# Optimization experiments

Hardware: AMD Instinct MI355X
Metric: run time of the kernel (lower is better)

Reference implementation:

```python
import jax, jax.numpy as jnp
import numpy as np

N = 100000   # points in input set
K = 1024     # num centroids AND max neighbors per ball (as in original code)
C = 64       # input feature channels
R = 0.2      # ball radius
LAYERS = (64, 64, 128)


def setup_inputs() -> dict:
    key = jax.random.key(0)
    ks = jax.random.split(key, 9)
    coords = jax.random.uniform(ks[0], (N, 3), dtype=jnp.float32)
    features = jax.random.normal(ks[1], (N, C), dtype=jnp.float32)
    centroid_idx = jax.random.randint(ks[2], (K,), 0, N)
    dims = (3 + C,) + LAYERS
    params = {}
    for i in range(len(LAYERS)):
        fin, fout = dims[i], dims[i + 1]
        params[f"W{i+1}"] = (jax.random.normal(ks[3 + i], (fin, fout), dtype=jnp.float32)
                             / np.float32(np.sqrt(fin)))
        params[f"b{i+1}"] = jax.random.normal(ks[6 + i], (fout,), dtype=jnp.float32) * 0.01
    return dict(coords=coords, features=features, centroid_idx=centroid_idx, **params)


def reference(coords, features, centroid_idx, W1, b1, W2, b2, W3, b3):
    cent = coords[centroid_idx]                                   # [K,3]
    # squared distances [K,N] without materializing [K,N,3]
    d2 = (jnp.sum(cent * cent, axis=-1)[:, None]
          + jnp.sum(coords * coords, axis=-1)[None, :]
          - 2.0 * cent @ coords.T)
    mask = d2 <= R * R                                            # ball query
    # take the FIRST K in-radius points in original index order (matches [:K])
    rank = jnp.cumsum(mask.astype(jnp.int32), axis=1) - 1
    sel = mask & (rank < K)
    order = jnp.where(sel, jnp.arange(N)[None, :], N)
    idx = jnp.sort(order, axis=1)[:, :K]                          # [K,K]
    valid = idx < N
    idx_c = jnp.minimum(idx, N - 1)
    rel = coords[idx_c] - cent[:, None, :]                        # centered coords
    x = jnp.concatenate([rel, features[idx_c]], axis=-1)          # [K,K,3+C]
    for W, b in ((W1, b1), (W2, b2), (W3, b3)):
        x = jax.nn.relu(x @ W + b)
    x = jnp.where(valid[:, :, None], x, -jnp.inf)
    new_features = jnp.max(x, axis=1)                             # per-region max pool
    return cent, new_features
```

## Files before the change

kernel.cpp:

```cpp
#include <hip/hip_runtime.h>
#include <hip/hip_bf16.h>

#define NPTS    100000
#define KCENT   1024
#define NSEG    391
#define NWORDS  1564
#define WSTRIDE 1600
#define MB_BLKS (NSEG*32)

typedef __attribute__((ext_vector_type(8))) short bf16x8;
typedef __attribute__((ext_vector_type(4))) float f32x4;
typedef unsigned long long u64;

__device__ __forceinline__ unsigned short f2bf(float x) {
  union { float f; unsigned u; } v; v.f = x;
  unsigned r = v.u + 0x7FFFu + ((v.u >> 16) & 1u);
  return (unsigned short)(r >> 16);
}
__device__ __forceinline__ unsigned pk2bf(float a, float b) {
  union { __hip_bfloat162 h; unsigned u; } cv;
  cv.h = __float22bfloat162_rn(make_float2(a, b));
  return cv.u;
}
__device__ __forceinline__ bf16x8 pack_bf8(f32x4 a, f32x4 b) {
  union { bf16x8 v; unsigned u[4]; } r;
  r.u[0] = pk2bf(a[0], a[1]); r.u[1] = pk2bf(a[2], a[3]);
  r.u[2] = pk2bf(b[0], b[1]); r.u[3] = pk2bf(b[2], b[3]);
  return r.v;
}

__global__ __launch_bounds__(256) void build_prep_kernel(
    const float* __restrict__ coords, const float* __restrict__ features,
    const int* __restrict__ cidx, const float* __restrict__ W1,
    const float* __restrict__ b1, const float* __restrict__ W2,
    const float* __restrict__ W3, u64* __restrict__ maskbuf,
    unsigned short* __restrict__ featsBF, f32x4* __restrict__ coords4,
    unsigned short* __restrict__ W1T, unsigned short* __restrict__ W2T,
    unsigned short* __restrict__ W3T, float* __restrict__ outCent) {
  const int bid = blockIdx.x;
  const int tid = threadIdx.x;
  if (bid < MB_BLKS) {
    const int grp = bid / NSEG, seg = bid - grp*NSEG;
    __shared__ float sC[96];
    __shared__ float sCC[32];
    if (tid < 96) sC[tid] = coords[cidx[grp*32 + tid/3]*3 + tid%3];
    __syncthreads();
    if (tid < 32) {
      float x = sC[tid*3], y = sC[tid*3+1], z = sC[tid*3+2];
      sCC[tid] = __fadd_rn(__fadd_rn(__fmul_rn(x,x), __fmul_rn(y,y)), __fmul_rn(z,z));
    }
    const int p = seg*256 + tid;
    const bool inr = p < NPTS;
    float px = 0.f, py = 0.f, pz = 0.f;
    if (inr) { px = coords[p*3]; py = coords[p*3+1]; pz = coords[p*3+2]; }
    const float pp = __fadd_rn(__fadd_rn(__fmul_rn(px,px), __fmul_rn(py,py)), __fmul_rn(pz,pz));
    __syncthreads();
    const int lane = tid & 63, wid = tid >> 6;
    u64 myw = 0ull;
    #pragma unroll
    for (int ci = 0; ci < 32; ++ci) {
      float cx = sC[ci*3], cy = sC[ci*3+1], cz = sC[ci*3+2];
      float dt = __fadd_rn(__fadd_rn(__fmul_rn(cx,px), __fmul_rn(cy,py)), __fmul_rn(cz,pz));
      float d2 = __fsub_rn(__fadd_rn(sCC[ci], pp), __fmul_rn(2.0f, dt));
      bool sel = inr && (d2 <= 0.04f);
      u64 m = __ballot(sel);
      if (lane == ci) myw = m;
    }
    if (lane < 32)
      maskbuf[(u64)(grp*32 + lane)*WSTRIDE + seg*4 + wid] = myw;
    return;
  }
  int i = (bid - MB_BLKS) * 256 + tid;
  if (i < 800000) {
    const f32x4* src = (const f32x4*)features + i*2;
    f32x4 f0 = src[0], f1 = src[1];
    union { bf16x8 v; uint4 u; } pk; pk.v = pack_bf8(f0, f1);
    ((uint4*)featsBF)[i] = pk.u;
    return;
  }
  i -= 800000;
  if (i < NPTS) {
    coords4[i] = (f32x4){coords[3*i], coords[3*i+1], coords[3*i+2], 0.f};
    return;
  }
  i -= NPTS;
  if (i < 6144) {
    int n = i / 96, kk = i - n*96;
    float v = 0.f;
    if (kk < 64)       v = W1[(3+kk)*64 + n];
    else if (kk < 67)  v = W1[(kk-64)*64 + n];
    else if (kk == 67) v = b1[n];
    W1T[n*96 + kk] = f2bf(v);
    return;
  }
  i -= 6144;
  if (i < 4608) { int n = i / 72, kk = i - n*72;
    W2T[n*72 + kk] = f2bf(kk < 64 ? W2[kk*64 + n] : 0.f); return; }
  i -= 4608;
  if (i < 9216) { int n = i / 72, kk = i - n*72;
    W3T[n*72 + kk] = f2bf(kk < 64 ? W3[kk*128 + n] : 0.f); return; }
  i -= 9216;
  if (i < KCENT) {
    int ci = cidx[i];
    outCent[i*3+0] = coords[ci*3+0];
    outCent[i*3+1] = coords[ci*3+1];
    outCent[i*3+2] = coords[ci*3+2];
  }
}

__global__ __launch_bounds__(256, 2) void fused_kernel(
    const u64* __restrict__ maskbuf, const unsigned short* __restrict__ featsBF,
    const f32x4* __restrict__ coords4, const float* __restrict__ cent,
    const float* __restrict__ b2v, const float* __restrict__ b3v,
    const unsigned short* __restrict__ gW1T, const unsigned short* __restrict__ gW2T,
    const unsigned short* __restrict__ gW3T, float* __restrict__ outF) {
  __shared__ __align__(16) unsigned short sW2T[64*72];
  __shared__ __align__(16) unsigned short sH[4*2*16*72];
  __shared__ int sIdx[KCENT];
  __shared__ int sTot[4];
  __shared__ float sB2[64], sB3[128];
  __shared__ float sMax[512];

  const int k = blockIdx.x;
  const int tid = threadIdx.x;
  const int w = tid >> 6, lane = tid & 63;
  const int q = lane >> 4, cl = lane & 15;

  const u64* M = maskbuf + (u64)k * WSTRIDE;
  u64 wv0 = M[tid], wv1 = M[256 + tid], wv2 = M[512 + tid];

  for (int i = tid; i < 576; i += 256) ((uint4*)sW2T)[i] = ((const uint4*)gW2T)[i];
  if (tid < 64)  sB2[tid] = b2v[tid];
  if (tid < 128) sB3[tid] = b3v[tid];

  bf16x8 w1f[3][4], w3f[2][8];
  #pragma unroll
  for (int ks = 0; ks < 3; ++ks)
    #pragma unroll
    for (int nt = 0; nt < 4; ++nt)
      w1f[ks][nt] = *(const bf16x8*)(gW1T + (nt*16+cl)*96 + ks*32 + q*8);
  #pragma unroll
  for (int ks = 0; ks < 2; ++ks)
    #pragma unroll
    for (int nt = 0; nt < 8; ++nt)
      w3f[ks][nt] = *(const bf16x8*)(gW3T + (nt*16+cl)*72 + ks*32 + q*8);

  int base = 0;
  #pragma unroll 1
  for (int r = 0; r < 7; ++r) {
    const int widx = r*256 + tid;
    u64 word = (r == 0) ? wv0 : (r == 1) ? wv1 : (r == 2) ? wv2
             : ((widx < NWORDS) ? M[widx] : 0ull);
    int pc = __popcll(word);
    int inc = pc;
    #pragma unroll
    for (int d = 1; d < 64; d <<= 1) {
      int t = __shfl_up(inc, d);
      if (lane >= d) inc += t;
    }
    if (lane == 63) sTot[w] = inc;
    __syncthreads();
    int wbase = 0, tot = 0;
    #pragma unroll
    for (int i = 0; i < 4; ++i) { int v = sTot[i]; tot += v; if (i < w) wbase += v; }
    int pos = base + wbase + inc - pc;
    const int pbase = widx * 64;
    while (word != 0ull && pos < KCENT) {
      int b = __ffsll(word) - 1;
      sIdx[pos++] = pbase + b;
      word &= word - 1ull;
    }
    base += tot;
    __syncthreads();
    if (base >= KCENT) break;
  }
  const int count = base < KCENT ? base : KCENT;

  const float cx = cent[k*3], cy = cent[k*3+1], cz = cent[k*3+2];
  unsigned short* myHA = sH + w*2304;
  unsigned short* myHB = myHA + 1152;

  f32x4 runmax[8];
  #pragma unroll
  for (int i = 0; i < 8; ++i)
    runmax[i] = (f32x4){-__builtin_inff(), -__builtin_inff(),
                        -__builtin_inff(), -__builtin_inff()};

  const int nstrips = (count + 15) >> 4;
  const int npairs  = (nstrips + 1) >> 1;
  int pp = w;

  int pA = 0, pB = 0;
  { int jA = 32*pp + cl;      if (jA < count) pA = sIdx[jA];
    int jB = 32*pp + 16 + cl; if (jB < count) pB = sIdx[jB]; }
  f32x4  c4A = coords4[pA], c4B = coords4[pB];
  bf16x8 xfA0 = *(const bf16x8*)(featsBF + pA*64 + q*8);
  bf16x8 xfA1 = *(const bf16x8*)(featsBF + pA*64 + 32 + q*8);
  bf16x8 xfB0 = *(const bf16x8*)(featsBF + pB*64 + q*8);
  bf16x8 xfB1 = *(const bf16x8*)(featsBF + pB*64 + 32 + q*8);
  int pA2 = 0, pB2 = 0;
  { int jA = 32*(pp+4) + cl;      if (jA < count) pA2 = sIdx[jA];
    int jB = 32*(pp+4) + 16 + cl; if (jB < count) pB2 = sIdx[jB]; }

  const bf16x8 zero8 = (bf16x8){0,0,0,0,0,0,0,0};

  for (; pp < npairs; pp += 4) {
    int pA3 = 0, pB3 = 0;
    { int jA = 32*(pp+8) + cl;      if (jA < count) pA3 = sIdx[jA];
      int jB = 32*(pp+8) + 16 + cl; if (jB < count) pB3 = sIdx[jB]; }

    union { bf16x8 v; unsigned u[4]; } rfA, rfB;
    rfA.u[0] = pk2bf(c4A[0]-cx, c4A[1]-cy); rfA.u[1] = pk2bf(c4A[2]-cz, 1.0f);
    rfA.u[2] = 0u; rfA.u[3] = 0u;
    rfB.u[0] = pk2bf(c4B[0]-cx, c4B[1]-cy); rfB.u[1] = pk2bf(c4B[2]-cz, 1.0f);
    rfB.u[2] = 0u; rfB.u[3] = 0u;
    bf16x8 x2A = (q == 0) ? rfA.v : zero8;
    bf16x8 x2B = (q == 0) ? rfB.v : zero8;

    {
      f32x4 accA[4], accB[4];
      #pragma unroll
      for (int nt = 0; nt < 4; ++nt) { accA[nt] = (f32x4){0.f,0.f,0.f,0.f};
                                       accB[nt] = (f32x4){0.f,0.f,0.f,0.f}; }
      #pragma unroll
      for (int nt = 0; nt < 4; ++nt) {
        accA[nt] = __builtin_amdgcn_mfma_f32_16x16x32_bf16(w1f[0][nt], xfA0, accA[nt], 0,0,0);
        accB[nt] = __builtin_amdgcn_mfma_f32_16x16x32_bf16(w1f[0][nt], xfB0, accB[nt], 0,0,0);
      }
      #pragma unroll
      for (int nt = 0; nt < 4; ++nt) {
        accA[nt] = __builtin_amdgcn_mfma_f32_16x16x32_bf16(w1f[1][nt], xfA1, accA[nt], 0,0,0);
        accB[nt] = __builtin_amdgcn_mfma_f32_16x16x32_bf16(w1f[1][nt], xfB1, accB[nt], 0,0,0);
      }
      #pragma unroll
      for (int nt = 0; nt < 4; ++nt) {
        accA[nt] = __builtin_amdgcn_mfma_f32_16x16x32_bf16(w1f[2][nt], x2A, accA[nt], 0,0,0);
        accB[nt] = __builtin_amdgcn_mfma_f32_16x16x32_bf16(w1f[2][nt], x2B, accB[nt], 0,0,0);
      }
      #pragma unroll
      for (int nt = 0; nt < 4; ++nt) {
        const int o = nt*16 + q*4;
        uint2 pkA = { pk2bf(fmaxf(accA[nt][0],0.f), fmaxf(accA[nt][1],0.f)),
                      pk2bf(fmaxf(accA[nt][2],0.f), fmaxf(accA[nt][3],0.f)) };
        *(uint2*)(myHA + cl*72 + o) = pkA;
        uint2 pkB = { pk2bf(fmaxf(accB[nt][0],0.f), fmaxf(accB[nt][1],0.f)),
                      pk2bf(fmaxf(accB[nt][2],0.f), fmaxf(accB[nt][3],0.f)) };
        *(uint2*)(myHB + cl*72 + o) = pkB;
      }
    }

    c4A = coords4[pA2]; c4B = coords4[pB2];
    xfA0 = *(const bf16x8*)(featsBF + pA2*64 + q*8);
    xfA1 = *(const bf16x8*)(featsBF + pA2*64 + 32 + q*8);
    xfB0 = *(const bf16x8*)(featsBF + pB2*64 + q*8);
    xfB1 = *(const bf16x8*)(featsBF + pB2*64 + 32 + q*8);

    {
      bf16x8 hA0 = *(const bf16x8*)(myHA + cl*72 + q*8);
      bf16x8 hA1 = *(const bf16x8*)(myHA + cl*72 + 32 + q*8);
      bf16x8 hB0 = *(const bf16x8*)(myHB + cl*72 + q*8);
      bf16x8 hB1 = *(const bf16x8*)(myHB + cl*72 + 32 + q*8);
      f32x4 accA[4], accB[4];
      #pragma unroll
      for (int nt = 0; nt < 4; ++nt) { accA[nt] = (f32x4){0.f,0.f,0.f,0.f};
                                       accB[nt] = (f32x4){0.f,0.f,0.f,0.f}; }
      #pragma unroll
      for (int nt = 0; nt < 4; ++nt) {
        const unsigned short* wrow = sW2T + (nt*16+cl)*72 + q*8;
        bf16x8 wa0 = *(const bf16x8*)(wrow);
        accA[nt] = __builtin_amdgcn_mfma_f32_16x16x32_bf16(wa0, hA0, accA[nt], 0,0,0);
        accB[nt] = __builtin_amdgcn_mfma_f32_16x16x32_bf16(wa0, hB0, accB[nt], 0,0,0);
        bf16x8 wa1 = *(const bf16x8*)(wrow + 32);
        accA[nt] = __builtin_amdgcn_mfma_f32_16x16x32_bf16(wa1, hA1, accA[nt], 0,0,0);
        accB[nt] = __builtin_amdgcn_mfma_f32_16x16x32_bf16(wa1, hB1, accB[nt], 0,0,0);
      }
      #pragma unroll
      for (int nt = 0; nt < 4; ++nt) {
        const int o = nt*16 + q*4;
        f32x4 bb = *(const f32x4*)(sB2 + o);
        uint2 pkA = { pk2bf(fmaxf(accA[nt][0]+bb[0],0.f), fmaxf(accA[nt][1]+bb[1],0.f)),
                      pk2bf(fmaxf(accA[nt][2]+bb[2],0.f), fmaxf(accA[nt][3]+bb[3],0.f)) };
        *(uint2*)(myHA + cl*72 + o) = pkA;
        uint2 pkB = { pk2bf(fmaxf(accB[nt][0]+bb[0],0.f), fmaxf(accB[nt][1]+bb[1],0.f)),
                      pk2bf(fmaxf(accB[nt][2]+bb[2],0.f), fmaxf(accB[nt][3]+bb[3],0.f)) };
        *(uint2*)(myHB + cl*72 + o) = pkB;
      }
    }

    {
      bf16x8 hA0 = *(const bf16x8*)(myHA + cl*72 + q*8);
      bf16x8 hA1 = *(const bf16x8*)(myHA + cl*72 + 32 + q*8);
      bf16x8 hB0 = *(const bf16x8*)(myHB + cl*72 + q*8);
      bf16x8 hB1 = *(const bf16x8*)(myHB + cl*72 + 32 + q*8);
      const float vmA = (32*pp + cl      < count) ? 0.f : -__builtin_inff();
      const float vmB = (32*pp + 16 + cl < count) ? 0.f : -__builtin_inff();
      f32x4 a3A[8], a3B[8];
      #pragma unroll
      for (int nt = 0; nt < 8; ++nt) { a3A[nt] = (f32x4){0.f,0.f,0.f,0.f};
                                       a3B[nt] = (f32x4){0.f,0.f,0.f,0.f}; }
      #pragma unroll
      for (int nt = 0; nt < 8; ++nt) {
        a3A[nt] = __builtin_amdgcn_mfma_f32_16x16x32_bf16(w3f[0][nt], hA0, a3A[nt], 0,0,0);
        a3B[nt] = __builtin_amdgcn_mfma_f32_16x16x32_bf16(w3f[0][nt], hB0, a3B[nt], 0,0,0);
      }
      #pragma unroll
      for (int nt = 0; nt < 8; ++nt) {
        a3A[nt] = __builtin_amdgcn_mfma_f32_16x16x32_bf16(w3f[1][nt], hA1, a3A[nt], 0,0,0);
        a3B[nt] = __builtin_amdgcn_mfma_f32_16x16x32_bf16(w3f[1][nt], hB1, a3B[nt], 0,0,0);
      }
      #pragma unroll
      for (int nt = 0; nt < 8; ++nt)
        #pragma unroll
        for (int r = 0; r < 4; ++r)
          runmax[nt][r] = fmaxf(runmax[nt][r],
                                fmaxf(a3A[nt][r] + vmA, a3B[nt][r] + vmB));
    }

    pA2 = pA3; pB2 = pB3;
  }

  #pragma unroll
  for (int nt = 0; nt < 8; ++nt) {
    #pragma unroll
    for (int r = 0; r < 4; ++r) {
      float m = runmax[nt][r];
      m = fmaxf(m, __shfl_xor(m, 1));
      m = fmaxf(m, __shfl_xor(m, 2));
      m = fmaxf(m, __shfl_xor(m, 4));
      m = fmaxf(m, __shfl_xor(m, 8));
      runmax[nt][r] = m;
    }
    if (cl == 0) *(f32x4*)(sMax + w*128 + nt*16 + q*4) = runmax[nt];
  }
  __syncthreads();
  if (tid < 128) {
    float m = fmaxf(fmaxf(sMax[tid], sMax[128+tid]),
                    fmaxf(sMax[256+tid], sMax[384+tid]));
    outF[k*128 + tid] = fmaxf(m + sB3[tid], 0.f);
  }
}

extern "C" void kernel_launch(void* const* d_in, const int* in_sizes, int n_in,
                              void* d_out, int out_size, void* d_ws, size_t ws_size,
                              hipStream_t stream) {
  const float* coords   = (const float*)d_in[0];
  const float* features = (const float*)d_in[1];
  const int*   cidx     = (const int*)d_in[2];
  const float* W1 = (const float*)d_in[3];
  const float* b1 = (const float*)d_in[4];
  const float* W2 = (const float*)d_in[5];
  const float* b2 = (const float*)d_in[6];
  const float* W3 = (const float*)d_in[7];
  const float* b3 = (const float*)d_in[8];
  float* out = (float*)d_out;

  char* ws = (char*)d_ws;
  u64* maskbuf            = (u64*)(ws + 0);
  unsigned short* featsBF = (unsigned short*)(ws + 13107200);
  f32x4* coords4          = (f32x4*)(ws + 25907200);
  unsigned short* W1T = (unsigned short*)(ws + 27507200);
  unsigned short* W2T = (unsigned short*)(ws + 27519488);
  unsigned short* W3T = (unsigned short*)(ws + 27528704);

  build_prep_kernel<<<MB_BLKS + 3598, 256, 0, stream>>>(
      coords, features, cidx, W1, b1, W2, W3,
      maskbuf, featsBF, coords4, W1T, W2T, W3T, out);
  fused_kernel<<<KCENT, 256, 0, stream>>>(
      maskbuf, featsBF, coords4, out, b2, b3,
      W1T, W2T, W3T, out + 3072);
}
```

Baseline: 219.4 us.

## Transpose ball-query mask layout to word-major and halve centroids per block

The ball-query bitmask buffer is stored word-major, indexed [word][centroid], instead of centroid-major. The mask-building blocks now handle 16 centroids each, so there are twice as many of them; each thread keeps its centroid coordinates in registers rather than shared memory. Mask words are staged in shared memory and written out as 128-byte contiguous runs, replacing the per-lane strided stores. The cost is that the fused kernel's per-thread mask reads now stride by 8 KB, so it relies on neighbouring centroid blocks sharing cache lines, and each point's coordinates are loaded twice as often.

```diff
diff --git a/kernel.cpp b/kernel.cpp
--- a/kernel.cpp
+++ b/kernel.cpp
@@ -5,8 +5,7 @@
 #define KCENT   1024
 #define NSEG    391
 #define NWORDS  1564
-#define WSTRIDE 1600
-#define MB_BLKS (NSEG*32)
+#define MB_BLKS (NSEG*64)
 
 typedef __attribute__((ext_vector_type(8))) short bf16x8;
 typedef __attribute__((ext_vector_type(4))) float f32x4;
@@ -41,33 +40,38 @@
   const int tid = threadIdx.x;
   if (bid < MB_BLKS) {
     const int grp = bid / NSEG, seg = bid - grp*NSEG;
-    __shared__ float sC[96];
-    __shared__ float sCC[32];
-    if (tid < 96) sC[tid] = coords[cidx[grp*32 + tid/3]*3 + tid%3];
-    __syncthreads();
-    if (tid < 32) {
-      float x = sC[tid*3], y = sC[tid*3+1], z = sC[tid*3+2];
-      sCC[tid] = __fadd_rn(__fadd_rn(__fmul_rn(x,x), __fmul_rn(y,y)), __fmul_rn(z,z));
+    __shared__ u64 sWords[64];
+    const int lane = tid & 63, wid = tid >> 6;
+    float cx[16], cy[16], cz[16], cc[16];
+    #pragma unroll
+    for (int j = 0; j < 16; ++j) {
+      int c = cidx[grp*16 + j];
+      cx[j] = coords[c*3]; cy[j] = coords[c*3+1]; cz[j] = coords[c*3+2];
+      cc[j] = __fadd_rn(__fadd_rn(__fmul_rn(cx[j],cx[j]), __fmul_rn(cy[j],cy[j])),
+                        __fmul_rn(cz[j],cz[j]));
     }
     const int p = seg*256 + tid;
     const bool inr = p < NPTS;
     float px = 0.f, py = 0.f, pz = 0.f;
     if (inr) { px = coords[p*3]; py = coords[p*3+1]; pz = coords[p*3+2]; }
-    const float pp = __fadd_rn(__fadd_rn(__fmul_rn(px,px), __fmul_rn(py,py)), __fmul_rn(pz,pz));
-    __syncthreads();
-    const int lane = tid & 63, wid = tid >> 6;
+    const float pp = __fadd_rn(__fadd_rn(__fmul_rn(px,px), __fmul_rn(py,py)),
+                               __fmul_rn(pz,pz));
     u64 myw = 0ull;
     #pragma unroll
-    for (int ci = 0; ci < 32; ++ci) {
-      float cx = sC[ci*3], cy = sC[ci*3+1], cz = sC[ci*3+2];
-      float dt = __fadd_rn(__fadd_rn(__fmul_rn(cx,px), __fmul_rn(cy,py)), __fmul_rn(cz,pz));
-      float d2 = __fsub_rn(__fadd_rn(sCC[ci], pp), __fmul_rn(2.0f, dt));
+    for (int ci = 0; ci < 16; ++ci) {
+      float dt = __fadd_rn(__fadd_rn(__fmul_rn(cx[ci],px), __fmul_rn(cy[ci],py)),
+                           __fmul_rn(cz[ci],pz));
+      float d2 = __fsub_rn(__fadd_rn(cc[ci], pp), __fmul_rn(2.0f, dt));
       bool sel = inr && (d2 <= 0.04f);
       u64 m = __ballot(sel);
       if (lane == ci) myw = m;
     }
-    if (lane < 32)
-      maskbuf[(u64)(grp*32 + lane)*WSTRIDE + seg*4 + wid] = myw;
+    if (lane < 16) sWords[wid*16 + lane] = myw;
+    __syncthreads();
+    if (tid < 64) {
+      int wwid = tid >> 4, ci = tid & 15;
+      maskbuf[(u64)(seg*4 + wwid)*1024 + grp*16 + ci] = sWords[wwid*16 + ci];
+    }
     return;
   }
   int i = (bid - MB_BLKS) * 256 + tid;
@@ -126,8 +130,9 @@
   const int w = tid >> 6, lane = tid & 63;
   const int q = lane >> 4, cl = lane & 15;
 
-  const u64* M = maskbuf + (u64)k * WSTRIDE;
-  u64 wv0 = M[tid], wv1 = M[256 + tid], wv2 = M[512 + tid];
+  u64 wv0 = maskbuf[(u64)tid*1024 + k];
+  u64 wv1 = maskbuf[(u64)(256 + tid)*1024 + k];
+  u64 wv2 = maskbuf[(u64)(512 + tid)*1024 + k];
 
   for (int i = tid; i < 576; i += 256) ((uint4*)sW2T)[i] = ((const uint4*)gW2T)[i];
   if (tid < 64)  sB2[tid] = b2v[tid];
@@ -150,7 +155,7 @@
   for (int r = 0; r < 7; ++r) {
     const int widx = r*256 + tid;
     u64 word = (r == 0) ? wv0 : (r == 1) ? wv1 : (r == 2) ? wv2
-             : ((widx < NWORDS) ? M[widx] : 0ull);
+             : ((widx < NWORDS) ? maskbuf[(u64)widx*1024 + k] : 0ull);
     int pc = __popcll(word);
     int inc = pc;
     #pragma unroll
```

Measured after the change: 226.2 us. +3.1%, slower.

## Move MLP weights to LDS and run 8 single-strip waves per block

Applied to the files above, without the earlier changes.

Layer 1 and layer 3 weights now sit in shared memory and are read per MFMA, where before they were held in registers. The block grows from 256 to 512 threads. Each wave now handles one 16-point strip instead of an interleaved A/B pair, and W1T is padded to a 104-element row stride. Register pressure drops so more waves can be resident to hide gather latency, at the cost of extra LDS traffic, less instruction-level parallelism per wave, and more LDS per block.

```diff
diff --git a/kernel.cpp b/kernel.cpp
--- a/kernel.cpp
+++ b/kernel.cpp
@@ -84,16 +84,16 @@
     return;
   }
   i -= NPTS;
-  if (i < 6144) {
-    int n = i / 96, kk = i - n*96;
+  if (i < 6656) {
+    int n = i / 104, kk = i - n*104;
     float v = 0.f;
     if (kk < 64)       v = W1[(3+kk)*64 + n];
     else if (kk < 67)  v = W1[(kk-64)*64 + n];
     else if (kk == 67) v = b1[n];
-    W1T[n*96 + kk] = f2bf(v);
+    W1T[n*104 + kk] = f2bf(v);
     return;
   }
-  i -= 6144;
+  i -= 6656;
   if (i < 4608) { int n = i / 72, kk = i - n*72;
     W2T[n*72 + kk] = f2bf(kk < 64 ? W2[kk*64 + n] : 0.f); return; }
   i -= 4608;
@@ -108,18 +108,20 @@
   }
 }
 
-__global__ __launch_bounds__(256, 2) void fused_kernel(
+__global__ __launch_bounds__(512, 4) void fused_kernel(
     const u64* __restrict__ maskbuf, const unsigned short* __restrict__ featsBF,
     const f32x4* __restrict__ coords4, const float* __restrict__ cent,
     const float* __restrict__ b2v, const float* __restrict__ b3v,
     const unsigned short* __restrict__ gW1T, const unsigned short* __restrict__ gW2T,
     const unsigned short* __restrict__ gW3T, float* __restrict__ outF) {
+  __shared__ __align__(16) unsigned short sW1T[64*104];
   __shared__ __align__(16) unsigned short sW2T[64*72];
-  __shared__ __align__(16) unsigned short sH[4*2*16*72];
+  __shared__ __align__(16) unsigned short sW3T[128*72];
+  __shared__ __align__(16) unsigned short sH[8*16*72];
   __shared__ int sIdx[KCENT];
-  __shared__ int sTot[4];
+  __shared__ int sTot[8];
   __shared__ float sB2[64], sB3[128];
-  __shared__ float sMax[512];
+  __shared__ float sMax[8*128];
 
   const int k = blockIdx.x;
   const int tid = threadIdx.x;
@@ -127,28 +129,22 @@
   const int q = lane >> 4, cl = lane & 15;
 
   const u64* M = maskbuf + (u64)k * WSTRIDE;
-  u64 wv0 = M[tid], wv1 = M[256 + tid], wv2 = M[512 + tid];
-
-  for (int i = tid; i < 576; i += 256) ((uint4*)sW2T)[i] = ((const uint4*)gW2T)[i];
+  u64 wv0 = M[tid];
+  u64 wv1 = (512  + tid < NWORDS) ? M[512  + tid] : 0ull;
+  u64 wv2 = (1024 + tid < NWORDS) ? M[1024 + tid] : 0ull;
+
+  for (int i = tid; i < 832;  i += 512) ((uint4*)sW1T)[i] = ((const uint4*)gW1T)[i];
+  for (int i = tid; i < 576;  i += 512) ((uint4*)sW2T)[i] = ((const uint4*)gW2T)[i];
+  for (int i = tid; i < 1152; i += 512) ((uint4*)sW3T)[i] = ((const uint4*)gW3T)[i];
   if (tid < 64)  sB2[tid] = b2v[tid];
-  if (tid < 128) sB3[tid] = b3v[tid];
-
-  bf16x8 w1f[3][4], w3f[2][8];
-  #pragma unroll
-  for (int ks = 0; ks < 3; ++ks)
-    #pragma unroll
-    for (int nt = 0; nt < 4; ++nt)
-      w1f[ks][nt] = *(const bf16x8*)(gW1T + (nt*16+cl)*96 + ks*32 + q*8);
-  #pragma unroll
-  for (int ks = 0; ks < 2; ++ks)
-    #pragma unroll
-    for (int nt = 0; nt < 8; ++nt)
-      w3f[ks][nt] = *(const bf16x8*)(gW3T + (nt*16+cl)*72 + ks*32 + q*8);
+  if (tid >= 64 && tid < 192) sB3[tid-64] = b3v[tid-64];
+
+  const float cx = cent[k*3], cy = cent[k*3+1], cz = cent[k*3+2];
 
   int base = 0;
   #pragma unroll 1
-  for (int r = 0; r < 7; ++r) {
-    const int widx = r*256 + tid;
+  for (int r = 0; r < 4; ++r) {
+    const int widx = r*512 + tid;
     u64 word = (r == 0) ? wv0 : (r == 1) ? wv1 : (r == 2) ? wv2
              : ((widx < NWORDS) ? M[widx] : 0ull);
     int pc = __popcll(word);
@@ -162,7 +158,7 @@
     __syncthreads();
     int wbase = 0, tot = 0;
     #pragma unroll
-    for (int i = 0; i < 4; ++i) { int v = sTot[i]; tot += v; if (i < w) wbase += v; }
+    for (int i = 0; i < 8; ++i) { int v = sTot[i]; tot += v; if (i < w) wbase += v; }
     int pos = base + wbase + inc - pc;
     const int pbase = widx * 64;
     while (word != 0ull && pos < KCENT) {
@@ -176,9 +172,7 @@
   }
   const int count = base < KCENT ? base : KCENT;
 
-  const float cx = cent[k*3], cy = cent[k*3+1], cz = cent[k*3+2];
-  unsigned short* myHA = sH + w*2304;
-  unsigned short* myHB = myHA + 1152;
+  unsigned short* myH = sH + w*1152;
 
   f32x4 runmax[8];
   #pragma unroll
@@ -187,136 +181,107 @@
                         -__builtin_inff(), -__builtin_inff()};
 
   const int nstrips = (count + 15) >> 4;
-  const int npairs  = (nstrips + 1) >> 1;
-  int pp = w;
-
-  int pA = 0, pB = 0;
-  { int jA = 32*pp + cl;      if (jA < count) pA = sIdx[jA];
-    int jB = 32*pp + 16 + cl; if (jB < count) pB = sIdx[jB]; }
-  f32x4  c4A = coords4[pA], c4B = coords4[pB];
-  bf16x8 xfA0 = *(const bf16x8*)(featsBF + pA*64 + q*8);
-  bf16x8 xfA1 = *(const bf16x8*)(featsBF + pA*64 + 32 + q*8);
-  bf16x8 xfB0 = *(const bf16x8*)(featsBF + pB*64 + q*8);
-  bf16x8 xfB1 = *(const bf16x8*)(featsBF + pB*64 + 32 + q*8);
-  int pA2 = 0, pB2 = 0;
-  { int jA = 32*(pp+4) + cl;      if (jA < count) pA2 = sIdx[jA];
-    int jB = 32*(pp+4) + 16 + cl; if (jB < count) pB2 = sIdx[jB]; }
+  int s = w;
+
+  int pC = 0;
+  { int j = 16*s + cl; if (j < count) pC = sIdx[j]; }
+  f32x4  c4 = coords4[pC];
+  bf16x8 xf0 = *(const bf16x8*)(featsBF + pC*64 + q*8);
+  bf16x8 xf1 = *(const bf16x8*)(featsBF + pC*64 + 32 + q*8);
+  int pN = 0;
+  { int j = 16*(s+8) + cl; if (j < count) pN = sIdx[j]; }
 
   const bf16x8 zero8 = (bf16x8){0,0,0,0,0,0,0,0};
 
-  for (; pp < npairs; pp += 4) {
-    int pA3 = 0, pB3 = 0;
-    { int jA = 32*(pp+8) + cl;      if (jA < count) pA3 = sIdx[jA];
-      int jB = 32*(pp+8) + 16 + cl; if (jB < count) pB3 = sIdx[jB]; }
-
-    union { bf16x8 v; unsigned u[4]; } rfA, rfB;
-    rfA.u[0] = pk2bf(c4A[0]-cx, c4A[1]-cy); rfA.u[1] = pk2bf(c4A[2]-cz, 1.0f);
-    rfA.u[2] = 0u; rfA.u[3] = 0u;
-    rfB.u[0] = pk2bf(c4B[0]-cx, c4B[1]-cy); rfB.u[1] = pk2bf(c4B[2]-cz, 1.0f);
-    rfB.u[2] = 0u; rfB.u[3] = 0u;
-    bf16x8 x2A = (q == 0) ? rfA.v : zero8;
-    bf16x8 x2B = (q == 0) ? rfB.v : zero8;
+  for (; s < nstrips; s += 8) {
+    int pNN = 0;
+    { int j = 16*(s+16) + cl; if (j < count) pNN = sIdx[j]; }
+
+    union { bf16x8 v; unsigned u[4]; } rf;
+    rf.u[0] = pk2bf(c4[0]-cx, c4[1]-cy); rf.u[1] = pk2bf(c4[2]-cz, 1.0f);
+    rf.u[2] = 0u; rf.u[3] = 0u;
+    bf16x8 x2 = (q == 0) ? rf.v : zero8;
 
     {
-      f32x4 accA[4], accB[4];
-      #pragma unroll
-      for (int nt = 0; nt < 4; ++nt) { accA[nt] = (f32x4){0.f,0.f,0.f,0.f};
-                                       accB[nt] = (f32x4){0.f,0.f,0.f,0.f}; }
+      f32x4 acc[4];
+      #pragma unroll
+      for (int nt = 0; nt < 4; ++nt) acc[nt] = (f32x4){0.f,0.f,0.f,0.f};
       #pragma unroll
       for (int nt = 0; nt < 4; ++nt) {
-        accA[nt] = __builtin_amdgcn_mfma_f32_16x16x32_bf16(w1f[0][nt], xfA0, accA[nt], 0,0,0);
-        accB[nt] = __builtin_amdgcn_mfma_f32_16x16x32_bf16(w1f[0][nt], xfB0, accB[nt], 0,0,0);
-      }
-      #pragma unroll
-      for (int nt = 0; nt < 4; ++nt) {
-        accA[nt] = __builtin_amdgcn_mfma_f32_16x16x32_bf16(w1f[1][nt], xfA1, accA[nt], 0,0,0);
-        accB[nt] = __builtin_amdgcn_mfma_f32_16x16x32_bf16(w1f[1][nt], xfB1, accB[nt], 0,0,0);
-      }
-      #pragma unroll
-      for (int nt = 0; nt < 4; ++nt) {
-        accA[nt] = __builtin_amdgcn_mfma_f32_16x16x32_bf16(w1f[2][nt], x2A, accA[nt], 0,0,0);
-        accB[nt] = __builtin_amdgcn_mfma_f32_16x16x32_bf16(w1f[2][nt], x2B, accB[nt], 0,0,0);
+        const unsigned short* wrow = sW1T + (nt*16+cl)*104 + q*8;
+        bf16x8 wa0 = *(const bf16x8*)(wrow);
+        acc[nt] = __builtin_amdgcn_mfma_f32_16x16x32_bf16(wa0, xf0, acc[nt], 0,0,0);
+        bf16x8 wa1 = *(const bf16x8*)(wrow + 32);
+        acc[nt] = __builtin_amdgcn_mfma_f32_16x16x32_bf16(wa1, xf1, acc[nt], 0,0,0);
+        bf16x8 wa2 = *(const bf16x8*)(wrow + 64);
+        acc[nt] = __builtin_amdgcn_mfma_f32_16x16x32_bf16(wa2, x2,  acc[nt], 0,0,0);
       }
       #pragma unroll
       for (int nt = 0; nt < 4; ++nt) {
         const int o = nt*16 + q*4;
-        uint2 pkA = { pk2bf(fmaxf(accA[nt][0],0.f), fmaxf(accA[nt][1],0.f)),
-                      pk2bf(fmaxf(accA[nt][2],0.f), fmaxf(accA[nt][3],0.f)) };
-        *(uint2*)(myHA + cl*72 + o) = pkA;
-        uint2 pkB = { pk2bf(fmaxf(accB[nt][0],0.f), fmaxf(accB[nt][1],0.f)),
-                      pk2bf(fmaxf(accB[nt][2],0.f), fmaxf(accB[nt][3],0.f)) };
-        *(uint2*)(myHB + cl*72 + o) = pkB;
-      }
-    }
-
-    c4A = coords4[pA2]; c4B = coords4[pB2];
-    xfA0 = *(const bf16x8*)(featsBF + pA2*64 + q*8);
-    xfA1 = *(const bf16x8*)(featsBF + pA2*64 + 32 + q*8);
-    xfB0 = *(const bf16x8*)(featsBF + pB2*64 + q*8);
-    xfB1 = *(const bf16x8*)(featsBF + pB2*64 + 32 + q*8);
+        uint2 pk = { pk2bf(fmaxf(acc[nt][0],0.f), fmaxf(acc[nt][1],0.f)),
+                     pk2bf(fmaxf(acc[nt][2],0.f), fmaxf(acc[nt][3],0.f)) };
+        *(uint2*)(myH + cl*72 + o) = pk;
+      }
+    }
+
+    c4 = coords4[pN];
+    xf0 = *(const bf16x8*)(featsBF + pN*64 + q*8);
+    xf1 = *(const bf16x8*)(featsBF + pN*64 + 32 + q*8);
 
     {
-      bf16x8 hA0 = *(const bf16x8*)(myHA + cl*72 + q*8);
-      bf16x8 hA1 = *(const bf16x8*)(myHA + cl*72 + 32 + q*8);
-      bf16x8 hB0 = *(const bf16x8*)(myHB + cl*72 + q*8);
-      bf16x8 hB1 = *(const bf16x8*)(myHB + cl*72 + 32 + q*8);
-      f32x4 accA[4], accB[4];
-      #pragma unroll
-      for (int nt = 0; nt < 4; ++nt) { accA[nt] = (f32x4){0.f,0.f,0.f,0.f};
-                                       accB[nt] = (f32x4){0.f,0.f,0.f,0.f}; }
+      bf16x8 h0 = *(const bf16x8*)(myH + cl*72 + q*8);
+      bf16x8 h1 = *(const bf16x8*)(myH + cl*72 + 32 + q*8);
+      f32x4 acc[4];
+      #pragma unroll
+      for (int nt = 0; nt < 4; ++nt) acc[nt] = (f32x4){0.f,0.f,0.f,0.f};
       #pragma unroll
       for (int nt = 0; nt < 4; ++nt) {
         const unsigned short* wrow = sW2T + (nt*16+cl)*72 + q*8;
         bf16x8 wa0 = *(const bf16x8*)(wrow);
-        accA[nt] = __builtin_amdgcn_mfma_f32_16x16x32_bf16(wa0, hA0, accA[nt], 0,0,0);
-        accB[nt] = __builtin_amdgcn_mfma_f32_16x16x32_bf16(wa0, hB0, accB[nt], 0,0,0);
+        acc[nt] = __builtin_amdgcn_mfma_f32_16x16x32_bf16(wa0, h0, acc[nt], 0,0,0);
         bf16x8 wa1 = *(const bf16x8*)(wrow + 32);
-        accA[nt] = __builtin_amdgcn_mfma_f32_16x16x32_bf16(wa1, hA1, accA[nt], 0,0,0);
-        accB[nt] = __builtin_amdgcn_mfma_f32_16x16x32_bf16(wa1, hB1, accB[nt], 0,0,0);
+        acc[nt] = __builtin_amdgcn_mfma_f32_16x16x32_bf16(wa1, h1, acc[nt], 0,0,0);
       }
       #pragma unroll
       for (int nt = 0; nt < 4; ++nt) {
         const int o = nt*16 + q*4;
         f32x4 bb = *(const f32x4*)(sB2 + o);
-        uint2 pkA = { pk2bf(fmaxf(accA[nt][0]+bb[0],0.f), fmaxf(accA[nt][1]+bb[1],0.f)),
-                      pk2bf(fmaxf(accA[nt][2]+bb[2],0.f), fmaxf(accA[nt][3]+bb[3],0.f)) };
-        *(uint2*)(myHA + cl*72 + o) = pkA;
-        uint2 pkB = { pk2bf(fmaxf(accB[nt][0]+bb[0],0.f), fmaxf(accB[nt][1]+bb[1],0.f)),
-                      pk2bf(fmaxf(accB[nt][2]+bb[2],0.f), fmaxf(accB[nt][3]+bb[3],0.f)) };
-        *(uint2*)(myHB + cl*72 + o) = pkB;
+        uint2 pk = { pk2bf(fmaxf(acc[nt][0]+bb[0],0.f), fmaxf(acc[nt][1]+bb[1],0.f)),
+                     pk2bf(fmaxf(acc[nt][2]+bb[2],0.f), fmaxf(acc[nt][3]+bb[3],0.f)) };
+        *(uint2*)(myH + cl*72 + o) = pk;
       }
     }
 
     {
-      bf16x8 hA0 = *(const bf16x8*)(myHA + cl*72 + q*8);
-      bf16x8 hA1 = *(const bf16x8*)(myHA + cl*72 + 32 + q*8);
-      bf16x8 hB0 = *(const bf16x8*)(myHB + cl*72 + q*8);
-      bf16x8 hB1 = *(const bf16x8*)(myHB + cl*72 + 32 + q*8);
-      const float vmA = (32*pp + cl      < count) ? 0.f : -__builtin_inff();
-      const float vmB = (32*pp + 16 + cl < count) ? 0.f : -__builtin_inff();
-      f32x4 a3A[8], a3B[8];
-      #pragma unroll
-      for (int nt = 0; nt < 8; ++nt) { a3A[nt] = (f32x4){0.f,0.f,0.f,0.f};
-                                       a3B[nt] = (f32x4){0.f,0.f,0.f,0.f}; }
-      #pragma unroll
-      for (int nt = 0; nt < 8; ++nt) {
-        a3A[nt] = __builtin_amdgcn_mfma_f32_16x16x32_bf16(w3f[0][nt], hA0, a3A[nt], 0,0,0);
-        a3B[nt] = __builtin_amdgcn_mfma_f32_16x16x32_bf16(w3f[0][nt], hB0, a3B[nt], 0,0,0);
-      }
-      #pragma unroll
-      for (int nt = 0; nt < 8; ++nt) {
-        a3A[nt] = __builtin_amdgcn_mfma_f32_16x16x32_bf16(w3f[1][nt], hA1, a3A[nt], 0,0,0);
-        a3B[nt] = __builtin_amdgcn_mfma_f32_16x16x32_bf16(w3f[1][nt], hB1, a3B[nt], 0,0,0);
-      }
-      #pragma unroll
-      for (int nt = 0; nt < 8; ++nt)
+      bf16x8 h0 = *(const bf16x8*)(myH + cl*72 + q*8);
+      bf16x8 h1 = *(const bf16x8*)(myH + cl*72 + 32 + q*8);
+      const float vm = (16*s + cl < count) ? 0.f : -__builtin_inff();
+      #pragma unroll
+      for (int ntq = 0; ntq < 4; ++ntq) {
+        f32x4 a3[2];
         #pragma unroll
-        for (int r = 0; r < 4; ++r)
-          runmax[nt][r] = fmaxf(runmax[nt][r],
-                                fmaxf(a3A[nt][r] + vmA, a3B[nt][r] + vmB));
-    }
-
-    pA2 = pA3; pB2 = pB3;
+        for (int j = 0; j < 2; ++j) a3[j] = (f32x4){0.f,0.f,0.f,0.f};
+        #pragma unroll
+        for (int j = 0; j < 2; ++j) {
+          const int nt = ntq*2 + j;
+          const unsigned short* wrow = sW3T + (nt*16+cl)*72 + q*8;
+          bf16x8 w30 = *(const bf16x8*)(wrow);
+          a3[j] = __builtin_amdgcn_mfma_f32_16x16x32_bf16(w30, h0, a3[j], 0,0,0);
+          bf16x8 w31 = *(const bf16x8*)(wrow + 32);
+          a3[j] = __builtin_amdgcn_mfma_f32_16x16x32_bf16(w31, h1, a3[j], 0,0,0);
+        }
+        #pragma unroll
+        for (int j = 0; j < 2; ++j) {
+          const int nt = ntq*2 + j;
+          #pragma unroll
+          for (int r = 0; r < 4; ++r)
+            runmax[nt][r] = fmaxf(runmax[nt][r], a3[j][r] + vm);
+        }
+      }
+    }
+
+    pN = pNN;
   }
 
   #pragma unroll
@@ -334,8 +299,9 @@
   }
   __syncthreads();
   if (tid < 128) {
-    float m = fmaxf(fmaxf(sMax[tid], sMax[128+tid]),
-                    fmaxf(sMax[256+tid], sMax[384+tid]));
+    float m = sMax[tid];
+    #pragma unroll
+    for (int i = 1; i < 8; ++i) m = fmaxf(m, sMax[i*128 + tid]);
     outF[k*128 + tid] = fmaxf(m + sB3[tid], 0.f);
   }
 }
@@ -359,13 +325,13 @@
   unsigned short* featsBF = (unsigned short*)(ws + 13107200);
   f32x4* coords4          = (f32x4*)(ws + 25907200);
   unsigned short* W1T = (unsigned short*)(ws + 27507200);
-  unsigned short* W2T = (unsigned short*)(ws + 27519488);
-  unsigned short* W3T = (unsigned short*)(ws + 27528704);
-
-  build_prep_kernel<<<MB_BLKS + 3598, 256, 0, stream>>>(
+  unsigned short* W2T = (unsigned short*)(ws + 27520512);
+  unsigned short* W3T = (unsigned short*)(ws + 27529728);
+
+  build_prep_kernel<<<MB_BLKS + 3600, 256, 0, stream>>>(
       coords, features, cidx, W1, b1, W2, W3,
       maskbuf, featsBF, coords4, W1T, W2T, W3T, out);
-  fused_kernel<<<KCENT, 256, 0, stream>>>(
+  fused_kernel<<<KCENT, 512, 0, stream>>>(
       maskbuf, featsBF, coords4, out, b2, b3,
       W1T, W2T, W3T, out + 3072);
 }
```

New measurement: 456.2 us. 108% more time.

## Precompute per-point layer-1 feature projection once and apply coord term in registers

Applied to the files above, without the earlier changes.

Splits layer 1 into a feature part (features·W1[3:]+b1), computed once per input point in the prep kernel with MFMA and stored as bf16, and a 3-wide relative-coordinate part applied with scalar FMAs inside the fused kernel. This removes the 24 per-pair layer-1 MFMAs, the LDS round trip for the hidden layer and the W1T register fragments, since layer-2 inputs now come straight from registers. It also splits the layer-3 accumulators into two halves to lower register pressure. In exchange, layer-1 MFMAs now run for all 100k points instead of only the gathered neighbors, and the precomputed pre-activation is rounded to bf16 before the coordinate term is added, which slightly changes numerics.

```diff
diff --git a/kernel.cpp b/kernel.cpp
--- a/kernel.cpp
+++ b/kernel.cpp
@@ -7,6 +7,7 @@
 #define NWORDS  1564
 #define WSTRIDE 1600
 #define MB_BLKS (NSEG*32)
+#define UG_BLKS 1563
 
 typedef __attribute__((ext_vector_type(8))) short bf16x8;
 typedef __attribute__((ext_vector_type(4))) float f32x4;
@@ -21,6 +22,9 @@
   union { __hip_bfloat162 h; unsigned u; } cv;
   cv.h = __float22bfloat162_rn(make_float2(a, b));
   return cv.u;
+}
+__device__ __forceinline__ float bf2f(unsigned short s) {
+  union { float f; unsigned u; } v; v.u = ((unsigned)s) << 16; return v.f;
 }
 __device__ __forceinline__ bf16x8 pack_bf8(f32x4 a, f32x4 b) {
   union { bf16x8 v; unsigned u[4]; } r;
@@ -34,9 +38,9 @@
     const int* __restrict__ cidx, const float* __restrict__ W1,
     const float* __restrict__ b1, const float* __restrict__ W2,
     const float* __restrict__ W3, u64* __restrict__ maskbuf,
-    unsigned short* __restrict__ featsBF, f32x4* __restrict__ coords4,
-    unsigned short* __restrict__ W1T, unsigned short* __restrict__ W2T,
-    unsigned short* __restrict__ W3T, float* __restrict__ outCent) {
+    unsigned short* __restrict__ uBF, f32x4* __restrict__ coords4,
+    unsigned short* __restrict__ W2T, unsigned short* __restrict__ W3T,
+    float* __restrict__ outCent) {
   const int bid = blockIdx.x;
   const int tid = threadIdx.x;
   if (bid < MB_BLKS) {
@@ -70,30 +74,65 @@
       maskbuf[(u64)(grp*32 + lane)*WSTRIDE + seg*4 + wid] = myw;
     return;
   }
-  int i = (bid - MB_BLKS) * 256 + tid;
-  if (i < 800000) {
-    const f32x4* src = (const f32x4*)features + i*2;
-    f32x4 f0 = src[0], f1 = src[1];
-    union { bf16x8 v; uint4 u; } pk; pk.v = pack_bf8(f0, f1);
-    ((uint4*)featsBF)[i] = pk.u;
+  if (bid < MB_BLKS + UG_BLKS) {
+    const int pbase = (bid - MB_BLKS) * 64;
+    __shared__ __align__(16) unsigned short sU[64*72];
+    __shared__ float sB1g[64];
+    const int w = tid >> 6, lane = tid & 63;
+    const int q = lane >> 4, cl = lane & 15;
+    if (tid < 64) sB1g[tid] = b1[tid];
+    bf16x8 wf[2][4];
+    #pragma unroll
+    for (int ks = 0; ks < 2; ++ks)
+      #pragma unroll
+      for (int nt = 0; nt < 4; ++nt) {
+        union { bf16x8 v; unsigned short s[8]; } t;
+        #pragma unroll
+        for (int i = 0; i < 8; ++i)
+          t.s[i] = f2bf(W1[(3 + ks*32 + q*8 + i)*64 + nt*16 + cl]);
+        wf[ks][nt] = t.v;
+      }
+    const int p = pbase + w*16 + cl;
+    const int ps = (p < NPTS) ? p : 0;
+    bf16x8 xb[2];
+    #pragma unroll
+    for (int ks = 0; ks < 2; ++ks) {
+      const float* fp = features + (u64)ps*64 + ks*32 + q*8;
+      xb[ks] = pack_bf8(*(const f32x4*)fp, *(const f32x4*)(fp + 4));
+    }
+    f32x4 acc[4];
+    #pragma unroll
+    for (int nt = 0; nt < 4; ++nt) acc[nt] = (f32x4){0.f,0.f,0.f,0.f};
+    #pragma unroll
+    for (int ks = 0; ks < 2; ++ks)
+      #pragma unroll
+      for (int nt = 0; nt < 4; ++nt)
+        acc[nt] = __builtin_amdgcn_mfma_f32_16x16x32_bf16(wf[ks][nt], xb[ks], acc[nt], 0,0,0);
+    __syncthreads();
+    #pragma unroll
+    for (int nt = 0; nt < 4; ++nt) {
+      const int o = nt*16 + q*4;
+      f32x4 bb = *(const f32x4*)(sB1g + o);
+      uint2 pk = { pk2bf(acc[nt][0]+bb[0], acc[nt][1]+bb[1]),
+                   pk2bf(acc[nt][2]+bb[2], acc[nt][3]+bb[3]) };
+      *(uint2*)(sU + (w*16+cl)*72 + o) = pk;
+    }
+    __syncthreads();
+    #pragma unroll
+    for (int it = 0; it < 2; ++it) {
+      int i = it*256 + tid;
+      int r = i >> 3, c = i & 7;
+      if (pbase + r < NPTS)
+        ((uint4*)(uBF + (u64)(pbase + r)*64))[c] = *(const uint4*)(sU + r*72 + c*8);
+    }
     return;
   }
-  i -= 800000;
+  int i = (bid - MB_BLKS - UG_BLKS) * 256 + tid;
   if (i < NPTS) {
     coords4[i] = (f32x4){coords[3*i], coords[3*i+1], coords[3*i+2], 0.f};
     return;
   }
   i -= NPTS;
-  if (i < 6144) {
-    int n = i / 96, kk = i - n*96;
-    float v = 0.f;
-    if (kk < 64)       v = W1[(3+kk)*64 + n];
-    else if (kk < 67)  v = W1[(kk-64)*64 + n];
-    else if (kk == 67) v = b1[n];
-    W1T[n*96 + kk] = f2bf(v);
-    return;
-  }
-  i -= 6144;
   if (i < 4608) { int n = i / 72, kk = i - n*72;
     W2T[n*72 + kk] = f2bf(kk < 64 ? W2[kk*64 + n] : 0.f); return; }
   i -= 4608;
@@ -109,15 +148,16 @@
 }
 
 __global__ __launch_bounds__(256, 2) void fused_kernel(
-    const u64* __restrict__ maskbuf, const unsigned short* __restrict__ featsBF,
+    const u64* __restrict__ maskbuf, const unsigned short* __restrict__ uBF,
     const f32x4* __restrict__ coords4, const float* __restrict__ cent,
-    const float* __restrict__ b2v, const float* __restrict__ b3v,
-    const unsigned short* __restrict__ gW1T, const unsigned short* __restrict__ gW2T,
+    const float* __restrict__ W1g, const float* __restrict__ b2v,
+    const float* __restrict__ b3v, const unsigned short* __restrict__ gW2T,
     const unsigned short* __restrict__ gW3T, float* __restrict__ outF) {
   __shared__ __align__(16) unsigned short sW2T[64*72];
   __shared__ __align__(16) unsigned short sH[4*2*16*72];
   __shared__ int sIdx[KCENT];
   __shared__ int sTot[4];
+  __shared__ float sW1a[192];
   __shared__ float sB2[64], sB3[128];
   __shared__ float sMax[512];
 
@@ -130,20 +170,18 @@
   u64 wv0 = M[tid], wv1 = M[256 + tid], wv2 = M[512 + tid];
 
   for (int i = tid; i < 576; i += 256) ((uint4*)sW2T)[i] = ((const uint4*)gW2T)[i];
+  if (tid < 192) sW1a[tid] = W1g[tid];
   if (tid < 64)  sB2[tid] = b2v[tid];
   if (tid < 128) sB3[tid] = b3v[tid];
 
-  bf16x8 w1f[3][4], w3f[2][8];
-  #pragma unroll
-  for (int ks = 0; ks < 3; ++ks)
-    #pragma unroll
-    for (int nt = 0; nt < 4; ++nt)
-      w1f[ks][nt] = *(const bf16x8*)(gW1T + (nt*16+cl)*96 + ks*32 + q*8);
+  bf16x8 w3f[2][8];
   #pragma unroll
   for (int ks = 0; ks < 2; ++ks)
     #pragma unroll
     for (int nt = 0; nt < 8; ++nt)
       w3f[ks][nt] = *(const bf16x8*)(gW3T + (nt*16+cl)*72 + ks*32 + q*8);
+
+  const float cx = cent[k*3], cy = cent[k*3+1], cz = cent[k*3+2];
 
   int base = 0;
   #pragma unroll 1
@@ -176,7 +214,15 @@
   }
   const int count = base < KCENT ? base : KCENT;
 
-  const float cx = cent[k*3], cy = cent[k*3+1], cz = cent[k*3+2];
+  float a00[8], a01[8], a10[8], a11[8], a20[8], a21[8];
+  #pragma unroll
+  for (int i = 0; i < 8; ++i) {
+    const int c0 = q*8 + i, c1 = 32 + q*8 + i;
+    a00[i] = sW1a[c0];       a01[i] = sW1a[c1];
+    a10[i] = sW1a[64 + c0];  a11[i] = sW1a[64 + c1];
+    a20[i] = sW1a[128 + c0]; a21[i] = sW1a[128 + c1];
+  }
+
   unsigned short* myHA = sH + w*2304;
   unsigned short* myHB = myHA + 1152;
 
@@ -194,72 +240,51 @@
   { int jA = 32*pp + cl;      if (jA < count) pA = sIdx[jA];
     int jB = 32*pp + 16 + cl; if (jB < count) pB = sIdx[jB]; }
   f32x4  c4A = coords4[pA], c4B = coords4[pB];
-  bf16x8 xfA0 = *(const bf16x8*)(featsBF + pA*64 + q*8);
-  bf16x8 xfA1 = *(const bf16x8*)(featsBF + pA*64 + 32 + q*8);
-  bf16x8 xfB0 = *(const bf16x8*)(featsBF + pB*64 + q*8);
-  bf16x8 xfB1 = *(const bf16x8*)(featsBF + pB*64 + 32 + q*8);
+  bf16x8 xfA0 = *(const bf16x8*)(uBF + pA*64 + q*8);
+  bf16x8 xfA1 = *(const bf16x8*)(uBF + pA*64 + 32 + q*8);
+  bf16x8 xfB0 = *(const bf16x8*)(uBF + pB*64 + q*8);
+  bf16x8 xfB1 = *(const bf16x8*)(uBF + pB*64 + 32 + q*8);
   int pA2 = 0, pB2 = 0;
   { int jA = 32*(pp+4) + cl;      if (jA < count) pA2 = sIdx[jA];
     int jB = 32*(pp+4) + 16 + cl; if (jB < count) pB2 = sIdx[jB]; }
-
-  const bf16x8 zero8 = (bf16x8){0,0,0,0,0,0,0,0};
 
   for (; pp < npairs; pp += 4) {
     int pA3 = 0, pB3 = 0;
     { int jA = 32*(pp+8) + cl;      if (jA < count) pA3 = sIdx[jA];
       int jB = 32*(pp+8) + 16 + cl; if (jB < count) pB3 = sIdx[jB]; }
 
-    union { bf16x8 v; unsigned u[4]; } rfA, rfB;
-    rfA.u[0] = pk2bf(c4A[0]-cx, c4A[1]-cy); rfA.u[1] = pk2bf(c4A[2]-cz, 1.0f);
-    rfA.u[2] = 0u; rfA.u[3] = 0u;
-    rfB.u[0] = pk2bf(c4B[0]-cx, c4B[1]-cy); rfB.u[1] = pk2bf(c4B[2]-cz, 1.0f);
-    rfB.u[2] = 0u; rfB.u[3] = 0u;
-    bf16x8 x2A = (q == 0) ? rfA.v : zero8;
-    bf16x8 x2B = (q == 0) ? rfB.v : zero8;
-
+    bf16x8 hbA0, hbA1, hbB0, hbB1;
     {
-      f32x4 accA[4], accB[4];
-      #pragma unroll
-      for (int nt = 0; nt < 4; ++nt) { accA[nt] = (f32x4){0.f,0.f,0.f,0.f};
-                                       accB[nt] = (f32x4){0.f,0.f,0.f,0.f}; }
-      #pragma unroll
-      for (int nt = 0; nt < 4; ++nt) {
-        accA[nt] = __builtin_amdgcn_mfma_f32_16x16x32_bf16(w1f[0][nt], xfA0, accA[nt], 0,0,0);
-        accB[nt] = __builtin_amdgcn_mfma_f32_16x16x32_bf16(w1f[0][nt], xfB0, accB[nt], 0,0,0);
+      const float rxA = c4A[0]-cx, ryA = c4A[1]-cy, rzA = c4A[2]-cz;
+      const float rxB = c4B[0]-cx, ryB = c4B[1]-cy, rzB = c4B[2]-cz;
+      union { bf16x8 v; unsigned short s[8]; } uA0, uA1, uB0, uB1;
+      uA0.v = xfA0; uA1.v = xfA1; uB0.v = xfB0; uB1.v = xfB1;
+      union { bf16x8 v; unsigned u[4]; } oA0, oA1, oB0, oB1;
+      #pragma unroll
+      for (int i = 0; i < 8; i += 2) {
+        float vA0a = bf2f(uA0.s[i])   + rxA*a00[i]   + ryA*a10[i]   + rzA*a20[i];
+        float vA0b = bf2f(uA0.s[i+1]) + rxA*a00[i+1] + ryA*a10[i+1] + rzA*a20[i+1];
+        oA0.u[i>>1] = pk2bf(fmaxf(vA0a, 0.f), fmaxf(vA0b, 0.f));
+        float vA1a = bf2f(uA1.s[i])   + rxA*a01[i]   + ryA*a11[i]   + rzA*a21[i];
+        float vA1b = bf2f(uA1.s[i+1]) + rxA*a01[i+1] + ryA*a11[i+1] + rzA*a21[i+1];
+        oA1.u[i>>1] = pk2bf(fmaxf(vA1a, 0.f), fmaxf(vA1b, 0.f));
+        float vB0a = bf2f(uB0.s[i])   + rxB*a00[i]   + ryB*a10[i]   + rzB*a20[i];
+        float vB0b = bf2f(uB0.s[i+1]) + rxB*a00[i+1] + ryB*a10[i+1] + rzB*a20[i+1];
+        oB0.u[i>>1] = pk2bf(fmaxf(vB0a, 0.f), fmaxf(vB0b, 0.f));
+        float vB1a = bf2f(uB1.s[i])   + rxB*a01[i]   + ryB*a11[i]   + rzB*a21[i];
+        float vB1b = bf2f(uB1.s[i+1]) + rxB*a01[i+1] + ryB*a11[i+1] + rzB*a21[i+1];
+        oB1.u[i>>1] = pk2bf(fmaxf(vB1a, 0.f), fmaxf(vB1b, 0.f));
       }
-      #pragma unroll
-      for (int nt = 0; nt < 4; ++nt) {
-        accA[nt] = __builtin_amdgcn_mfma_f32_16x16x32_bf16(w1f[1][nt], xfA1, accA[nt], 0,0,0);
-        accB[nt] = __builtin_amdgcn_mfma_f32_16x16x32_bf16(w1f[1][nt], xfB1, accB[nt], 0,0,0);
-      }
-      #pragma unroll
-      for (int nt = 0; nt < 4; ++nt) {
-        accA[nt] = __builtin_amdgcn_mfma_f32_16x16x32_bf16(w1f[2][nt], x2A, accA[nt], 0,0,0);
-        accB[nt] = __builtin_amdgcn_mfma_f32_16x16x32_bf16(w1f[2][nt], x2B, accB[nt], 0,0,0);
-      }
-      #pragma unroll
-      for (int nt = 0; nt < 4; ++nt) {
-        const int o = nt*16 + q*4;
-        uint2 pkA = { pk2bf(fmaxf(accA[nt][0],0.f), fmaxf(accA[nt][1],0.f)),
-                      pk2bf(fmaxf(accA[nt][2],0.f), fmaxf(accA[nt][3],0.f)) };
-        *(uint2*)(myHA + cl*72 + o) = pkA;
-        uint2 pkB = { pk2bf(fmaxf(accB[nt][0],0.f), fmaxf(accB[nt][1],0.f)),
-                      pk2bf(fmaxf(accB[nt][2],0.f), fmaxf(accB[nt][3],0.f)) };
-        *(uint2*)(myHB + cl*72 + o) = pkB;
-      }
+      hbA0 = oA0.v; hbA1 = oA1.v; hbB0 = oB0.v; hbB1 = oB1.v;
     }
 
     c4A = coords4[pA2]; c4B = coords4[pB2];
-    xfA0 = *(const bf16x8*)(featsBF + pA2*64 + q*8);
-    xfA1 = *(const bf16x8*)(featsBF + pA2*64 + 32 + q*8);
-    xfB0 = *(const bf16x8*)(featsBF + pB2*64 + q*8);
-    xfB1 = *(const bf16x8*)(featsBF + pB2*64 + 32 + q*8);
+    xfA0 = *(const bf16x8*)(uBF + pA2*64 + q*8);
+    xfA1 = *(const bf16x8*)(uBF + pA2*64 + 32 + q*8);
+    xfB0 = *(const bf16x8*)(uBF + pB2*64 + q*8);
+    xfB1 = *(const bf16x8*)(uBF + pB2*64 + 32 + q*8);
 
     {
-      bf16x8 hA0 = *(const bf16x8*)(myHA + cl*72 + q*8);
-      bf16x8 hA1 = *(const bf16x8*)(myHA + cl*72 + 32 + q*8);
-      bf16x8 hB0 = *(const bf16x8*)(myHB + cl*72 + q*8);
-      bf16x8 hB1 = *(const bf16x8*)(myHB + cl*72 + 32 + q*8);
       f32x4 accA[4], accB[4];
       #pragma unroll
       for (int nt = 0; nt < 4; ++nt) { accA[nt] = (f32x4){0.f,0.f,0.f,0.f};
@@ -268,11 +293,11 @@
       for (int nt = 0; nt < 4; ++nt) {
         const unsigned short* wrow = sW2T + (nt*16+cl)*72 + q*8;
         bf16x8 wa0 = *(const bf16x8*)(wrow);
-        accA[nt] = __builtin_amdgcn_mfma_f32_16x16x32_bf16(wa0, hA0, accA[nt], 0,0,0);
-        accB[nt] = __builtin_amdgcn_mfma_f32_16x16x32_bf16(wa0, hB0, accB[nt], 0,0,0);
+        accA[nt] = __builtin_amdgcn_mfma_f32_16x16x32_bf16(wa0, hbA0, accA[nt], 0,0,0);
+        accB[nt] = __builtin_amdgcn_mfma_f32_16x16x32_bf16(wa0, hbB0, accB[nt], 0,0,0);
         bf16x8 wa1 = *(const bf16x8*)(wrow + 32);
-        accA[nt] = __builtin_amdgcn_mfma_f32_16x16x32_bf16(wa1, hA1, accA[nt], 0,0,0);
-        accB[nt] = __builtin_amdgcn_mfma_f32_16x16x32_bf16(wa1, hB1, accB[nt], 0,0,0);
+        accA[nt] = __builtin_amdgcn_mfma_f32_16x16x32_bf16(wa1, hbA1, accA[nt], 0,0,0);
+        accB[nt] = __builtin_amdgcn_mfma_f32_16x16x32_bf16(wa1, hbB1, accB[nt], 0,0,0);
       }
       #pragma unroll
       for (int nt = 0; nt < 4; ++nt) {
@@ -294,26 +319,33 @@
       bf16x8 hB1 = *(const bf16x8*)(myHB + cl*72 + 32 + q*8);
       const float vmA = (32*pp + cl      < count) ? 0.f : -__builtin_inff();
       const float vmB = (32*pp + 16 + cl < count) ? 0.f : -__builtin_inff();
-      f32x4 a3A[8], a3B[8];
-      #pragma unroll
-      for (int nt = 0; nt < 8; ++nt) { a3A[nt] = (f32x4){0.f,0.f,0.f,0.f};
-                                       a3B[nt] = (f32x4){0.f,0.f,0.f,0.f}; }
-      #pragma unroll
-      for (int nt = 0; nt < 8; ++nt) {
-        a3A[nt] = __builtin_amdgcn_mfma_f32_16x16x32_bf16(w3f[0][nt], hA0, a3A[nt], 0,0,0);
-        a3B[nt] = __builtin_amdgcn_mfma_f32_16x16x32_bf16(w3f[0][nt], hB0, a3B[nt], 0,0,0);
+      #pragma unroll
+      for (int half = 0; half < 2; ++half) {
+        f32x4 a3A[4], a3B[4];
+        #pragma unroll
+        for (int j = 0; j < 4; ++j) { a3A[j] = (f32x4){0.f,0.f,0.f,0.f};
+                                      a3B[j] = (f32x4){0.f,0.f,0.f,0.f}; }
+        #pragma unroll
+        for (int j = 0; j < 4; ++j) {
+          const int nt = half*4 + j;
+          a3A[j] = __builtin_amdgcn_mfma_f32_16x16x32_bf16(w3f[0][nt], hA0, a3A[j], 0,0,0);
+          a3B[j] = __builtin_amdgcn_mfma_f32_16x16x32_bf16(w3f[0][nt], hB0, a3B[j], 0,0,0);
+        }
+        #pragma unroll
+        for (int j = 0; j < 4; ++j) {
+          const int nt = half*4 + j;
+          a3A[j] = __builtin_amdgcn_mfma_f32_16x16x32_bf16(w3f[1][nt], hA1, a3A[j], 0,0,0);
+          a3B[j] = __builtin_amdgcn_mfma_f32_16x16x32_bf16(w3f[1][nt], hB1, a3B[j], 0,0,0);
+        }
+        #pragma unroll
+        for (int j = 0; j < 4; ++j) {
+          const int nt = half*4 + j;
+          #pragma unroll
+          for (int r = 0; r < 4; ++r)
+            runmax[nt][r] = fmaxf(runmax[nt][r],
+                                  fmaxf(a3A[j][r] + vmA, a3B[j][r] + vmB));
+        }
       }
-      #pragma unroll
-      for (int nt = 0; nt < 8; ++nt) {
-        a3A[nt] = __builtin_amdgcn_mfma_f32_16x16x32_bf16(w3f[1][nt], hA1, a3A[nt], 0,0,0);
-        a3B[nt] = __builtin_amdgcn_mfma_f32_16x16x32_bf16(w3f[1][nt], hB1, a3B[nt], 0,0,0);
-      }
-      #pragma unroll
-      for (int nt = 0; nt < 8; ++nt)
-        #pragma unroll
-        for (int r = 0; r < 4; ++r)
-          runmax[nt][r] = fmaxf(runmax[nt][r],
-                                fmaxf(a3A[nt][r] + vmA, a3B[nt][r] + vmB));
     }
 
     pA2 = pA3; pB2 = pB3;
@@ -355,17 +387,16 @@
   float* out = (float*)d_out;
 
   char* ws = (char*)d_ws;
-  u64* maskbuf            = (u64*)(ws + 0);
-  unsigned short* featsBF = (unsigned short*)(ws + 13107200);
-  f32x4* coords4          = (f32x4*)(ws + 25907200);
-  unsigned short* W1T = (unsigned short*)(ws + 27507200);
-  unsigned short* W2T = (unsigned short*)(ws + 27519488);
-  unsigned short* W3T = (unsigned short*)(ws + 27528704);
-
-  build_prep_kernel<<<MB_BLKS + 3598, 256, 0, stream>>>(
+  u64* maskbuf        = (u64*)(ws + 0);
+  unsigned short* uBF = (unsigned short*)(ws + 13107200);
+  f32x4* coords4      = (f32x4*)(ws + 25907200);
+  unsigned short* W2T = (unsigned short*)(ws + 27507200);
+  unsigned short* W3T = (unsigned short*)(ws + 27516416);
+
+  build_prep_kernel<<<MB_BLKS + UG_BLKS + 449, 256, 0, stream>>>(
       coords, features, cidx, W1, b1, W2, W3,
-      maskbuf, featsBF, coords4, W1T, W2T, W3T, out);
+      maskbuf, uBF, coords4, W2T, W3T, out);
   fused_kernel<<<KCENT, 256, 0, stream>>>(
-      maskbuf, featsBF, coords4, out, b2, b3,
-      W1T, W2T, W3T, out + 3072);
-}
+      maskbuf, uBF, coords4, out, W1, b2, b3,
+      W2T, W3T, out + 3072);
+}
```

Measured after the change: 253.0 us. 15.3% more time.
